# Kernel optimization log

Measured on AMD Instinct MI355X. Metric: run time of the kernel, lower is better.

Reference implementation:

```python
import jax, jax.numpy as jnp
import numpy as np

H = 16
DH = 64
THETA = 10000.0


def setup_inputs() -> dict:
    key = jax.random.key(0)
    ks = jax.random.split(key, 9)
    B, M, R = 4, 1024, 256
    d = H * DH
    s = 0.05
    return {
        "Pq": jax.random.normal(ks[0], (B, M, R), jnp.float32) * s,
        "Pk": jax.random.normal(ks[1], (B, M, R), jnp.float32) * s,
        "Pv": jax.random.normal(ks[2], (B, M, R), jnp.float32) * s,
        "Vq": jax.random.normal(ks[3], (R, d), jnp.float32) * s,
        "Vk": jax.random.normal(ks[4], (R, d), jnp.float32) * s,
        "Vv": jax.random.normal(ks[5], (R, d), jnp.float32) * s,
        "bq": jax.random.normal(ks[6], (d,), jnp.float32) * s,
        "bk": jax.random.normal(ks[7], (d,), jnp.float32) * s,
        "bv": jax.random.normal(ks[8], (d,), jnp.float32) * s,
        "attention_mask": jnp.ones((B, M), jnp.int32),
        "position_ids": jnp.tile(jnp.arange(M, dtype=jnp.int32), (B, 1)),
    }


def _rope_cos_sin(position_ids):
    # half-dim frequencies, matching the kernel's half-half rotation
    half = DH // 2
    inv_freq = 1.0 / (THETA ** (jnp.arange(0, half, dtype=jnp.float32) / half))
    ang = position_ids.astype(jnp.float32)[..., None] * inv_freq  # [B,M,half]
    return jnp.cos(ang), jnp.sin(ang)


def _rotate(x, cos, sin):
    # x: [B,H,M,dh]; cos/sin: [B,M,half] -> broadcast over heads
    half = DH // 2
    x0, x1 = x[..., :half], x[..., half:]
    c = cos[:, None, :, :]
    s = sin[:, None, :, :]
    return jnp.concatenate([x0 * c - x1 * s, x0 * s + x1 * c], axis=-1)


def reference(Pq, Pk, Pv, Vq, Vk, Vv, bq, bk, bv, attention_mask, position_ids):
    B, M, R = Pq.shape
    # reconstruct per-head Q/K/V from low-rank factors
    Vq3 = Vq.reshape(R, H, DH)
    Vk3 = Vk.reshape(R, H, DH)
    Vv3 = Vv.reshape(R, H, DH)
    q = jnp.einsum("bmr,rhd->bhmd", Pq, Vq3) + bq.reshape(H, DH)[None, :, None, :]
    k = jnp.einsum("bmr,rhd->bhmd", Pk, Vk3) + bk.reshape(H, DH)[None, :, None, :]
    v = jnp.einsum("bmr,rhd->bhmd", Pv, Vv3) + bv.reshape(H, DH)[None, :, None, :]
    cos, sin = _rope_cos_sin(position_ids)
    q = _rotate(q, cos, sin)
    k = _rotate(k, cos, sin)
    scale = 1.0 / jnp.sqrt(jnp.float32(DH))
    scores = jnp.einsum("bhmd,bhnd->bhmn", q, k) * scale  # [B,H,M,M]
    valid = attention_mask.astype(bool)
    pad = valid[:, None, :, None] & valid[:, None, None, :]
    scores = jnp.where(pad, scores, -jnp.inf)
    p = jax.nn.softmax(scores, axis=-1)
    out = jnp.einsum("bhmn,bhnd->bhmd", p, v)
    return out
```

## Files before the change

### kernel.cpp

```cpp
#include <hip/hip_runtime.h>
#include <hip/hip_bf16.h>
#include <math.h>

#define BB 4
#define MM 1024
#define RR 256
#define HH 16
#define DHH 64
#define DD (HH*DHH)

typedef __attribute__((ext_vector_type(8))) short short8;
typedef __attribute__((ext_vector_type(4))) float f32x4;

static __device__ __forceinline__ unsigned short f2bf(float x) {
    __hip_bfloat16 h = __float2bfloat16(x);
    return *(unsigned short*)&h;
}

#if defined(__has_builtin)
#  if __has_builtin(__builtin_amdgcn_exp2f)
#    define EXP2F(x) __builtin_amdgcn_exp2f(x)
#  endif
#endif
#ifndef EXP2F
#  define EXP2F(x) __expf((x) * 0.6931471805599453f)
#endif

static __device__ __forceinline__ unsigned pack_bf16_rh(float a, float b) {
    unsigned ua = __builtin_bit_cast(unsigned, a) + 0x8000u;
    unsigned ub = __builtin_bit_cast(unsigned, b) + 0x8000u;
    return __builtin_amdgcn_perm(ub, ua, 0x07060302u);
}

__global__ __launch_bounds__(256) void prep_kernel(
    const float* __restrict__ Pq, const float* __restrict__ Pk, const float* __restrict__ Pv,
    const float* __restrict__ Vq, const float* __restrict__ Vk, const float* __restrict__ Vv,
    __hip_bfloat16* __restrict__ VTq, __hip_bfloat16* __restrict__ VTk,
    __hip_bfloat16* __restrict__ VTv, __hip_bfloat16* __restrict__ Pb)
{
    const int t = threadIdx.x;
    if (blockIdx.x < 768) {
        const int z   = blockIdx.x / 256;
        const int rem = blockIdx.x % 256;
        const int r0  = (rem & 7) * 32;
        const int d0  = (rem >> 3) * 32;
        const float* V = (z == 0) ? Vq : (z == 1) ? Vk : Vv;
        __hip_bfloat16* VT = (z == 0) ? VTq : (z == 1) ? VTk : VTv;

        __shared__ __hip_bfloat16 Ts[32][33];
        {
            const int row = t >> 3;
            const int c4  = (t & 7) * 4;
            float4 f = *(const float4*)&V[(size_t)(r0 + row) * DD + d0 + c4];
            Ts[row][c4 + 0] = __float2bfloat16(f.x);
            Ts[row][c4 + 1] = __float2bfloat16(f.y);
            Ts[row][c4 + 2] = __float2bfloat16(f.z);
            Ts[row][c4 + 3] = __float2bfloat16(f.w);
        }
        __syncthreads();
        {
            const int orow = t >> 3;
            const int oc4  = (t & 7) * 4;
            union { unsigned short u[4]; uint2 v; } pk;
            #pragma unroll
            for (int i = 0; i < 4; ++i) pk.u[i] = *(unsigned short*)&Ts[oc4 + i][orow];
            *(uint2*)&VT[(size_t)(d0 + orow) * RR + r0 + oc4] = pk.v;
        }
    } else {
        const size_t n4 = (size_t)BB * MM * RR / 4;
        size_t i = (size_t)(blockIdx.x - 768) * 256 + t;
        const int which = (int)(i / n4);
        const size_t off = i - (size_t)which * n4;
        const float* P = (which == 0) ? Pq : (which == 1) ? Pk : Pv;
        float4 f = *(const float4*)(P + off * 4);
        union { unsigned short u[4]; uint2 v; } pk;
        pk.u[0] = f2bf(f.x); pk.u[1] = f2bf(f.y); pk.u[2] = f2bf(f.z); pk.u[3] = f2bf(f.w);
        *(uint2*)((unsigned short*)Pb + (size_t)which * BB * MM * RR + off * 4) = pk.v;
    }
}

__global__ __launch_bounds__(256) void svd_gemm(
    const __hip_bfloat16* __restrict__ Pb,
    const __hip_bfloat16* __restrict__ VTq, const __hip_bfloat16* __restrict__ VTk,
    const __hip_bfloat16* __restrict__ VTv,
    const float* __restrict__ bq, const float* __restrict__ bk, const float* __restrict__ bv,
    const int* __restrict__ pos_ids,
    __hip_bfloat16* __restrict__ qout, __hip_bfloat16* __restrict__ kout,
    __hip_bfloat16* __restrict__ vTout)
{
    const int which = blockIdx.z;
    const short* P = (const short*)Pb + (size_t)which * BB * MM * RR;
    const __hip_bfloat16* VT = (which == 0) ? VTq : (which == 1) ? VTk : VTv;
    const float* bias        = (which == 0) ? bq : (which == 1) ? bk : bv;

    const int h   = blockIdx.y;
    const int bm0 = blockIdx.x * 256;
    const int b   = bm0 >> 10;
    const int m0  = bm0 & 1023;
    const int tid = threadIdx.x;
    const int lane = tid & 63;
    const int w    = tid >> 6;
    const int l15  = lane & 15;
    const int quad = lane >> 4;

    __shared__ alignas(16) short SM[256 * 72 + 64 * 72];
    short* As = SM;
    short* Bs = SM + 256 * 72;

    f32x4 acc[4][4];
    #pragma unroll
    for (int mt = 0; mt < 4; ++mt)
        #pragma unroll
        for (int dt = 0; dt < 4; ++dt) acc[mt][dt] = (f32x4){0.f, 0.f, 0.f, 0.f};

    for (int kc = 0; kc < 4; ++kc) {
        #pragma unroll
        for (int i = 0; i < 8; ++i) {
            int u = tid + i * 256;
            int row = u >> 3;
            int cg  = (u & 7) * 8;
            *(uint4*)&As[row * 72 + cg] =
                *(const uint4*)&P[(size_t)(bm0 + row) * RR + kc * 64 + cg];
        }
        #pragma unroll
        for (int i = 0; i < 2; ++i) {
            int u = tid + i * 256;
            int row = u >> 3;
            int cg  = (u & 7) * 8;
            *(uint4*)&Bs[row * 72 + cg] =
                *(const uint4*)((const short*)VT + (size_t)(h * 64 + row) * RR + kc * 64 + cg);
        }
        __syncthreads();

        #pragma unroll
        for (int ks = 0; ks < 2; ++ks) {
            short8 a[4];
            #pragma unroll
            for (int mt = 0; mt < 4; ++mt)
                a[mt] = *(const short8*)&As[(w * 64 + mt * 16 + l15) * 72 + ks * 32 + quad * 8];
            #pragma unroll
            for (int dt = 0; dt < 4; ++dt) {
                short8 bf = *(const short8*)&Bs[(dt * 16 + l15) * 72 + ks * 32 + quad * 8];
                #pragma unroll
                for (int mt = 0; mt < 4; ++mt)
                    acc[mt][dt] = __builtin_amdgcn_mfma_f32_16x16x32_bf16(a[mt], bf, acc[mt][dt], 0, 0, 0);
            }
        }
        __syncthreads();
    }

    #pragma unroll
    for (int dt = 0; dt < 4; ++dt) {
        float bc = bias[h * 64 + dt * 16 + l15];
        #pragma unroll
        for (int mt = 0; mt < 4; ++mt)
            #pragma unroll
            for (int r = 0; r < 4; ++r) acc[mt][dt][r] += bc;
    }

    if (which < 2) {
        __hip_bfloat16* out = (which == 0) ? qout : kout;
        int pm[4][4];
        #pragma unroll
        for (int mt = 0; mt < 4; ++mt)
            #pragma unroll
            for (int r = 0; r < 4; ++r)
                pm[mt][r] = pos_ids[bm0 + w * 64 + mt * 16 + quad * 4 + r];
        float cB[2][4][4], sB[2][4][4];
        #pragma unroll
        for (int f2 = 0; f2 < 2; ++f2) {
            float invf = __powf(10000.0f, -(float)(f2 * 16 + l15) * (1.0f / 32.0f));
            #pragma unroll
            for (int mt = 0; mt < 4; ++mt)
                #pragma unroll
                for (int r = 0; r < 4; ++r) {
                    float ang = (float)pm[mt][r] * invf;
                    __sincosf(ang, &sB[f2][mt][r], &cB[f2][mt][r]);
                }
        }
        #pragma unroll
        for (int dt = 0; dt < 4; ++dt) {
            const int cd = dt * 16 + l15;
            const int f2 = dt & 1;
            #pragma unroll
            for (int mt = 0; mt < 4; ++mt)
                #pragma unroll
                for (int r = 0; r < 4; ++r) {
                    float x  = acc[mt][dt][r];
                    float xp = acc[mt][dt ^ 2][r];
                    float c = cB[f2][mt][r], s = sB[f2][mt][r];
                    float val = (dt < 2) ? (x * c - xp * s) : (xp * s + x * c);
                    int m = m0 + w * 64 + mt * 16 + quad * 4 + r;
                    out[(((size_t)b * HH + h) * MM + m) * DHH + cd] = __float2bfloat16(val);
                }
        }
    } else {
        short* Tt = SM;
        __syncthreads();
        #pragma unroll
        for (int dt = 0; dt < 4; ++dt)
            #pragma unroll
            for (int mt = 0; mt < 4; ++mt) {
                union { unsigned short u[4]; uint2 v; } pk;
                #pragma unroll
                for (int r = 0; r < 4; ++r) pk.u[r] = f2bf(acc[mt][dt][r]);
                *(uint2*)&Tt[(dt * 16 + l15) * 264 + w * 64 + mt * 16 + quad * 4] = pk.v;
            }
        __syncthreads();
        #pragma unroll
        for (int it = 0; it < 8; ++it) {
            int u = tid + it * 256;
            int row = u >> 5;
            int seg = u & 31;
            *(uint4*)&vTout[(((size_t)b * HH + h) * DHH + row) * MM + m0 + seg * 8] =
                *(const uint4*)&Tt[row * 264 + seg * 8];
        }
    }
}

__global__ __launch_bounds__(256, 4) void attn_kernel(
    const __hip_bfloat16* __restrict__ q, const __hip_bfloat16* __restrict__ k,
    const __hip_bfloat16* __restrict__ vT,
    const int* __restrict__ mask, float* __restrict__ out)
{
    const int bh   = blockIdx.x & 63;
    const int qt   = blockIdx.x >> 6;
    const int b    = bh >> 4;
    const int tid  = threadIdx.x;
    const int lane = tid & 63;
    const int w    = tid >> 6;
    const int l15  = lane & 15;
    const int quad = lane >> 4;
    const int q0   = qt * 64;

    __shared__ alignas(16) __hip_bfloat16 Kt[128][72];
    __shared__ alignas(16) __hip_bfloat16 Vt[64][136];

    const short* kbase = (const short*)k  + (size_t)bh * MM * DHH;
    const short* vbase = (const short*)vT + (size_t)bh * DHH * MM;

    short8 qa[2];
    {
        const short* qb = (const short*)q +
            ((size_t)bh * MM + q0 + w * 16 + l15) * DHH + quad * 8;
        qa[0] = *(const short8*)(qb);
        qa[1] = *(const short8*)(qb + 32);
    }

    f32x4 Ot[4];
    #pragma unroll
    for (int dt = 0; dt < 4; ++dt) Ot[dt] = (f32x4){0.f, 0.f, 0.f, 0.f};
    float lsum = 0.f;

    const int* maskb = mask + b * MM;
    const int srcbase = (lane & 48) | ((lane & 48) >> 2);
    const float k2 = 0.125f * 1.44269504089f;

    for (int nc = 0; nc < MM / 128; ++nc) {
        const int n0 = nc * 128;
        #pragma unroll
        for (int pass = 0; pass < 4; ++pass) {
            int u   = tid + pass * 256;
            int row = u >> 3;
            int cg  = u & 7;
            *(uint4*)&Kt[row][cg * 8] =
                *(const uint4*)(kbase + (size_t)(n0 + row) * DHH + cg * 8);
        }
        #pragma unroll
        for (int pass = 0; pass < 4; ++pass) {
            int u   = tid + pass * 256;
            int row = u >> 4;
            int c   = u & 15;
            union { uint4 q4; uint2 h2[2]; } vld;
            vld.q4 = *(const uint4*)(vbase + (size_t)row * MM + n0 + c * 8);
            int g  = c >> 3;
            int c6 = c & 7;
            int base0 = g * 64 + (c6 >> 2) * 32 + (c6 & 1) * 16 + ((c6 >> 1) & 1) * 4;
            *(uint2*)&Vt[row][base0]     = vld.h2[0];
            *(uint2*)&Vt[row][base0 + 8] = vld.h2[1];
        }
        __syncthreads();

        unsigned long long bal0 = __ballot(maskb[n0 + lane] != 0);
        unsigned long long bal1 = __ballot(maskb[n0 + 64 + lane] != 0);

        f32x4 S[8];
        #pragma unroll
        for (int t = 0; t < 8; ++t) {
            const short* kr = (const short*)&Kt[t * 16 + l15][quad * 8];
            short8 ka0 = *(const short8*)(kr);
            short8 ka1 = *(const short8*)(kr + 32);
            f32x4 c = (f32x4){0.f, 0.f, 0.f, 0.f};
            c = __builtin_amdgcn_mfma_f32_16x16x32_bf16(ka0, qa[0], c, 0, 0, 0);
            c = __builtin_amdgcn_mfma_f32_16x16x32_bf16(ka1, qa[1], c, 0, 0, 0);
            S[t] = c;
        }

        #pragma unroll
        for (int t = 0; t < 8; ++t) {
            unsigned bits = (unsigned)((t < 4 ? bal0 : bal1) >> ((t & 3) * 16 + quad * 4));
            #pragma unroll
            for (int r = 0; r < 4; ++r) {
                float sb = ((bits >> r) & 1u) ? 0.0f : -1e30f;
                float e = EXP2F(fmaf(S[t][r], k2, sb));
                lsum += e;
                S[t][r] = e;
            }
        }

        short8 pa[4];
        #pragma unroll
        for (int p = 0; p < 4; ++p) {
            union { unsigned u[4]; short8 s; } pk;
            pk.u[0] = pack_bf16_rh(S[2*p][0],   S[2*p][1]);
            pk.u[1] = pack_bf16_rh(S[2*p][2],   S[2*p][3]);
            pk.u[2] = pack_bf16_rh(S[2*p+1][0], S[2*p+1][1]);
            pk.u[3] = pack_bf16_rh(S[2*p+1][2], S[2*p+1][3]);
            pa[p] = pk.s;
        }

        #pragma unroll
        for (int p = 0; p < 4; ++p) {
            #pragma unroll
            for (int dt = 0; dt < 4; ++dt) {
                short8 vb = *(const short8*)&Vt[dt * 16 + l15][p * 32 + quad * 8];
                Ot[dt] = __builtin_amdgcn_mfma_f32_16x16x32_bf16(pa[p], vb, Ot[dt], 0, 0, 0);
            }
        }
        __syncthreads();
    }

    {
        float s = lsum;
        s += __shfl_xor(s, 16, 64);
        s += __shfl_xor(s, 32, 64);
        float inv = 1.0f / s;
        float* ob = out + ((size_t)bh * MM + q0 + w * 16) * DHH;
        #pragma unroll
        for (int r = 0; r < 4; ++r) {
            float ir = __shfl(inv, srcbase + r, 64);
            #pragma unroll
            for (int dt = 0; dt < 4; ++dt)
                ob[(quad * 4 + r) * DHH + dt * 16 + l15] = Ot[dt][r] * ir;
        }
    }
}

extern "C" void kernel_launch(void* const* d_in, const int* in_sizes, int n_in,
                              void* d_out, int out_size, void* d_ws, size_t ws_size,
                              hipStream_t stream) {
    const float* Pq = (const float*)d_in[0];
    const float* Pk = (const float*)d_in[1];
    const float* Pv = (const float*)d_in[2];
    const float* Vq = (const float*)d_in[3];
    const float* Vk = (const float*)d_in[4];
    const float* Vv = (const float*)d_in[5];
    const float* bq = (const float*)d_in[6];
    const float* bk = (const float*)d_in[7];
    const float* bv = (const float*)d_in[8];
    const int* mask = (const int*)d_in[9];
    const int* pos  = (const int*)d_in[10];
    float* out = (float*)d_out;

    const size_t qkv_elems = (size_t)BB * HH * MM * DHH;
    __hip_bfloat16* qb  = (__hip_bfloat16*)d_ws;
    __hip_bfloat16* kb  = qb + qkv_elems;
    __hip_bfloat16* vT  = kb + qkv_elems;
    __hip_bfloat16* VTq = vT + qkv_elems;
    __hip_bfloat16* VTk = VTq + (size_t)DD * RR;
    __hip_bfloat16* VTv = VTk + (size_t)DD * RR;
    __hip_bfloat16* Pb  = VTv + (size_t)DD * RR;

    prep_kernel<<<768 + 3 * BB * MM * RR / 4 / 256, 256, 0, stream>>>(
        Pq, Pk, Pv, Vq, Vk, Vv, VTq, VTk, VTv, Pb);

    dim3 gG(BB * MM / 256, HH, 3);
    svd_gemm<<<gG, 256, 0, stream>>>(Pb, VTq, VTk, VTv, bq, bk, bv, pos, qb, kb, vT);

    attn_kernel<<<BB * HH * (MM / 64), 256, 0, stream>>>(qb, kb, vT, mask, out);
}
```

Measured before the change: 142.5 us.

## Load K and V fragments directly from global memory, dropping LDS staging

Removes the shared-memory staging of K and V tiles and the two block barriers per chunk, so each wave reads its MFMA operands straight from global memory (through cache). This gets rid of LDS writes, reads and synchronisation. In exchange, the four waves in a block each fetch the same K/V data redundantly, and the V reads become narrow 8-byte gathers, which raises global/L2 traffic and latency exposure.

Result: slower. 275.9 us (+93.5%).

```diff
diff --git a/kernel.cpp b/kernel.cpp
--- a/kernel.cpp
+++ b/kernel.cpp
@@ -233,9 +233,6 @@
     const int quad = lane >> 4;
     const int q0   = qt * 64;
 
-    __shared__ alignas(16) __hip_bfloat16 Kt[128][72];
-    __shared__ alignas(16) __hip_bfloat16 Vt[64][136];
-
     const short* kbase = (const short*)k  + (size_t)bh * MM * DHH;
     const short* vbase = (const short*)vT + (size_t)bh * DHH * MM;
 
@@ -256,30 +253,11 @@
     const int srcbase = (lane & 48) | ((lane & 48) >> 2);
     const float k2 = 0.125f * 1.44269504089f;
 
+    const short* krow0 = kbase + (size_t)l15 * DHH + quad * 8;
+    const short* vrow0 = vbase + (size_t)l15 * MM + quad * 4;
+
     for (int nc = 0; nc < MM / 128; ++nc) {
         const int n0 = nc * 128;
-        #pragma unroll
-        for (int pass = 0; pass < 4; ++pass) {
-            int u   = tid + pass * 256;
-            int row = u >> 3;
-            int cg  = u & 7;
-            *(uint4*)&Kt[row][cg * 8] =
-                *(const uint4*)(kbase + (size_t)(n0 + row) * DHH + cg * 8);
-        }
-        #pragma unroll
-        for (int pass = 0; pass < 4; ++pass) {
-            int u   = tid + pass * 256;
-            int row = u >> 4;
-            int c   = u & 15;
-            union { uint4 q4; uint2 h2[2]; } vld;
-            vld.q4 = *(const uint4*)(vbase + (size_t)row * MM + n0 + c * 8);
-            int g  = c >> 3;
-            int c6 = c & 7;
-            int base0 = g * 64 + (c6 >> 2) * 32 + (c6 & 1) * 16 + ((c6 >> 1) & 1) * 4;
-            *(uint2*)&Vt[row][base0]     = vld.h2[0];
-            *(uint2*)&Vt[row][base0 + 8] = vld.h2[1];
-        }
-        __syncthreads();
 
         unsigned long long bal0 = __ballot(maskb[n0 + lane] != 0);
         unsigned long long bal1 = __ballot(maskb[n0 + 64 + lane] != 0);
@@ -287,7 +265,7 @@
         f32x4 S[8];
         #pragma unroll
         for (int t = 0; t < 8; ++t) {
-            const short* kr = (const short*)&Kt[t * 16 + l15][quad * 8];
+            const short* kr = krow0 + (size_t)(n0 + t * 16) * DHH;
             short8 ka0 = *(const short8*)(kr);
             short8 ka1 = *(const short8*)(kr + 32);
             f32x4 c = (f32x4){0.f, 0.f, 0.f, 0.f};
@@ -323,11 +301,13 @@
         for (int p = 0; p < 4; ++p) {
             #pragma unroll
             for (int dt = 0; dt < 4; ++dt) {
-                short8 vb = *(const short8*)&Vt[dt * 16 + l15][p * 32 + quad * 8];
-                Ot[dt] = __builtin_amdgcn_mfma_f32_16x16x32_bf16(pa[p], vb, Ot[dt], 0, 0, 0);
+                const short* vr = vrow0 + (size_t)dt * 16 * MM + n0 + p * 32;
+                union { uint2 h2[2]; short8 s; } vb;
+                vb.h2[0] = *(const uint2*)(vr);
+                vb.h2[1] = *(const uint2*)(vr + 16);
+                Ot[dt] = __builtin_amdgcn_mfma_f32_16x16x32_bf16(pa[p], vb.s, Ot[dt], 0, 0, 0);
             }
         }
-        __syncthreads();
     }
 
     {
```
